# Performance work log

Hardware: AMD Instinct MI355X
Metric: run time of the kernel (lower is better)

## Reference

```python
import jax, jax.numpy as jnp
import numpy as np

DIM = 512
HEADS = 8
DIM_HEAD = 64
HIDDEN = HEADS * DIM_HEAD  # 512
B = 4
L = 2048
SCALE = DIM_HEAD ** -0.5


def setup_inputs() -> dict:
    key = jax.random.key(0)
    k1, k2, k3, k4 = jax.random.split(key, 4)
    x = jax.random.normal(k1, (B, DIM, L), dtype=jnp.float32)
    # Conv1d with kernel_size=1 == pointwise matmul over channels; store as [out, in]
    w_qkv = jax.random.normal(k2, (HIDDEN * 3, DIM), dtype=jnp.float32) * (DIM ** -0.5)
    w_out = jax.random.normal(k3, (DIM, HIDDEN), dtype=jnp.float32) * (HIDDEN ** -0.5)
    b_out = jax.random.normal(k4, (DIM,), dtype=jnp.float32) * 0.01
    return {"x": x, "w_qkv": w_qkv, "w_out": w_out, "b_out": b_out}


def reference(x, w_qkv, w_out, b_out):
    # x: [B, dim, L]
    qkv = jnp.einsum('oi,bil->bol', w_qkv, x)           # [B, 3*hidden, L]
    q, k, v = jnp.split(qkv, 3, axis=1)                  # each [B, hidden, L]

    def to_heads(t):
        # 'b (h c) l -> b h l c'
        return t.reshape(t.shape[0], HEADS, DIM_HEAD, t.shape[-1]).transpose(0, 1, 3, 2)

    q = to_heads(q) * SCALE                              # [B, H, L, c]
    k = to_heads(k)
    v = to_heads(v)

    attn = jax.nn.softmax(jnp.einsum('bhqc,bhkc->bhqk', q, k), axis=-1)  # [B,H,L,L]
    o = jnp.einsum('bhqk,bhkc->bhqc', attn, v)           # [B, H, L, c]
    o = o.transpose(0, 1, 3, 2).reshape(o.shape[0], HIDDEN, o.shape[2] if False else L)
    # 'b h c l -> b (h c) l' done via transpose+reshape above
    out = jnp.einsum('oi,bil->bol', w_out, o) + b_out[None, :, None]
    return out
```

## Files before the change

kernel.cpp:

```cpp
#include <hip/hip_runtime.h>

typedef unsigned short u16;
typedef __bf16 bf16x8 __attribute__((ext_vector_type(8)));
typedef float f32x4 __attribute__((ext_vector_type(4)));

#define B_ 4
#define L_ 2048
#define LOG2E 1.44269504088896340736f
#define HSTRIDE ((size_t)L_ * 64)

__device__ __forceinline__ u16 f2bf(float f) {
    unsigned u = __float_as_uint(f);
    u += 0x7fff + ((u >> 16) & 1);
    return (u16)(u >> 16);
}

__device__ __forceinline__ unsigned pk2(float a, float b) {
    return __builtin_amdgcn_perm(__float_as_uint(b), __float_as_uint(a), 0x07060302u);
}

__device__ __forceinline__ f32x4 mfma16(bf16x8 a, bf16x8 b, f32x4 c) {
    return __builtin_amdgcn_mfma_f32_16x16x32_bf16(a, b, c, 0, 0, 0);
}

__device__ __forceinline__ void async16(const u16* g, u16* l) {
    __builtin_amdgcn_global_load_lds(
        (const __attribute__((address_space(1))) u16*)g,
        (__attribute__((address_space(3))) u16*)l, 16, 0, 0);
}

__global__ __launch_bounds__(256) void convert_f32_bf16(const float* __restrict__ in,
                                                        u16* __restrict__ out, int n) {
    int i = (blockIdx.x * 256 + threadIdx.x) * 4;
    if (i < n) {
        float4 f = *(const float4*)(in + i);
        ushort4 r;
        r.x = f2bf(f.x); r.y = f2bf(f.y); r.z = f2bf(f.z); r.w = f2bf(f.w);
        *(ushort4*)(out + i) = r;
    }
}

__global__ __launch_bounds__(256) void transpose_x(const float* __restrict__ x,
                                                   u16* __restrict__ xbt) {
    __shared__ u16 T[64][66];
    int b  = blockIdx.z;
    int i0 = blockIdx.y * 64;
    int l0 = blockIdx.x * 64;
    int t  = threadIdx.x;
    int c  = t & 63, r4 = t >> 6;
    const float* xb = x + ((size_t)b * 512 + i0) * 2048 + l0;
#pragma unroll
    for (int r = r4; r < 64; r += 4) T[r][c] = f2bf(xb[(size_t)r * 2048 + c]);
    __syncthreads();
    u16* ob = xbt + ((size_t)b * 2048 + l0) * 512 + i0;
#pragma unroll
    for (int r = r4; r < 64; r += 4) ob[(size_t)r * 512 + c] = T[c][r];
}

__global__ __launch_bounds__(256, 2) void qkv_gemm(const u16* __restrict__ xbt,
                                                   const u16* __restrict__ wq,
                                                   u16* __restrict__ qkv) {
    __shared__ u16 smem[16384];
    u16* As = smem;
    u16* Bs = smem + 8192;
    int b  = blockIdx.z;
    int m0 = blockIdx.x * 128;
    int n0 = blockIdx.y * 128;
    int tid = threadIdx.x;
    int lane = tid & 63, wid = tid >> 6;
    int quad = lane >> 4, n15 = lane & 15;
    const u16* Abase = xbt + ((size_t)b * L_ + m0) * 512;
    const u16* Bbase = wq + (size_t)n0 * 512;
    int mw = (wid & 1) * 64, nw = (wid >> 1) * 64;
    f32x4 acc[4][4] = {};
    for (int k0 = 0; k0 < 512; k0 += 64) {
        __syncthreads();
#pragma unroll
        for (int c = 0; c < 4; ++c) {
            int off = wid * 2048 + c * 512 + lane * 8;
            int row = off >> 6, col = off & 63;
            async16(Abase + (size_t)row * 512 + k0 + col, As + wid * 2048 + c * 512);
            async16(Bbase + (size_t)row * 512 + k0 + col, Bs + wid * 2048 + c * 512);
        }
        __syncthreads();
#pragma unroll
        for (int ks = 0; ks < 2; ++ks) {
            bf16x8 af[4], bfr[4];
#pragma unroll
            for (int i = 0; i < 4; ++i)
                af[i] = *(const bf16x8*)&As[(mw + i * 16 + n15) * 64 + ks * 32 + quad * 8];
#pragma unroll
            for (int j = 0; j < 4; ++j)
                bfr[j] = *(const bf16x8*)&Bs[(nw + j * 16 + n15) * 64 + ks * 32 + quad * 8];
#pragma unroll
            for (int i = 0; i < 4; ++i)
#pragma unroll
                for (int j = 0; j < 4; ++j)
                    acc[i][j] = mfma16(af[i], bfr[j], acc[i][j]);
        }
    }
    if (n0 < 512) {
#pragma unroll
        for (int i = 0; i < 4; ++i) {
#pragma unroll
            for (int j = 0; j < 4; ++j) {
                int o = n0 + nw + j * 16 + n15;
                int h = (o >> 6) & 7, cc = o & 63;
                u16* dst = qkv + ((size_t)b * 3 * 8 + h) * HSTRIDE + cc;
#pragma unroll
                for (int r = 0; r < 4; ++r) {
                    int l = m0 + mw + i * 16 + quad * 4 + r;
                    dst[(size_t)l * 64] = f2bf(acc[i][j][r] * (0.125f * LOG2E));
                }
            }
        }
    } else if (n0 < 1024) {
#pragma unroll
        for (int i = 0; i < 4; ++i) {
            int tile = (m0 + mw + i * 16) >> 4;
#pragma unroll
            for (int j = 0; j < 4; ++j) {
                int o = n0 + nw + j * 16 + n15;
                int h = (o >> 6) & 7, c = o & 63;
                int ks_k = c >> 5, qk = (c >> 3) & 3, jj = c & 7;
                u16* dst = qkv + (((size_t)b * 3 + 1) * 8 + h) * HSTRIDE
                         + ((size_t)tile * 2 + ks_k) * 512 + qk * 128 + jj;
#pragma unroll
                for (int r = 0; r < 4; ++r) {
                    int n15k = quad * 4 + r;
                    dst[n15k * 8] = f2bf(acc[i][j][r]);
                }
            }
        }
    } else {
        int kt = m0 >> 7;
        u16* Vf = qkv + ((size_t)b * 3 + 2) * 8 * HSTRIDE;
#pragma unroll
        for (int i = 0; i < 4; ++i) {
            int L0 = mw + i * 16;
            int ks2 = (L0 >> 5) & 3;
            int r3 = ((L0 >> 3) + (quad >> 1)) & 3;
#pragma unroll
            for (int j = 0; j < 4; ++j) {
                int oo = (n0 - 1024) + nw + j * 16 + n15;
                int h = oo >> 6, c = oo & 63;
                ushort4 pk;
                pk.x = f2bf(acc[i][j][0]); pk.y = f2bf(acc[i][j][1]);
                pk.z = f2bf(acc[i][j][2]); pk.w = f2bf(acc[i][j][3]);
                *(ushort4*)&Vf[(size_t)h * HSTRIDE + kt * 8192 + ks2 * 2048
                               + (c >> 4) * 512 + r3 * 128 + n15 * 8 + (quad & 1) * 4] = pk;
            }
        }
    }
}

__global__ __launch_bounds__(256, 4) void attn_kernel(const u16* __restrict__ qkv,
                                                      u16* __restrict__ o2) {
    __shared__ u16 Ps[4 * 32 * 68];
    __shared__ float Ls[4][32];
    int bh = blockIdx.y;
    int b = bh >> 3, h = bh & 7;
    int q0 = blockIdx.x * 32;
    int tid = threadIdx.x, lane = tid & 63, wid = tid >> 6;
    int quad = lane >> 4, n15 = lane & 15;
    const u16* Qp = qkv + (((size_t)b * 3 + 0) * 8 + h) * HSTRIDE;
    const u16* Kf = qkv + (((size_t)b * 3 + 1) * 8 + h) * HSTRIDE;
    const u16* Vf = qkv + (((size_t)b * 3 + 2) * 8 + h) * HSTRIDE;
    u16* Pw = Ps + wid * (32 * 68);

    bf16x8 aq[2][2];
#pragma unroll
    for (int mf = 0; mf < 2; ++mf)
#pragma unroll
        for (int ks = 0; ks < 2; ++ks)
            aq[mf][ks] = *(const bf16x8*)
                &Qp[(size_t)(q0 + mf * 16 + n15) * 64 + ks * 32 + quad * 8];

    f32x4 oacc[2][4] = {};
    float lsumT[2] = {0.f, 0.f};

    for (int it = 0; it < 8; ++it) {
        int tile0 = wid * 32 + it * 4;
#pragma unroll
        for (int nf = 0; nf < 4; ++nf) {
            const u16* kb = Kf + (size_t)(tile0 + nf) * 1024;
            bf16x8 ak0 = *(const bf16x8*)&kb[lane * 8];
            bf16x8 ak1 = *(const bf16x8*)&kb[512 + lane * 8];
#pragma unroll
            for (int mf = 0; mf < 2; ++mf) {
                f32x4 sT = {};
                sT = mfma16(ak0, aq[mf][0], sT);
                sT = mfma16(ak1, aq[mf][1], sT);
                float p0 = __builtin_amdgcn_exp2f(sT[0]);
                float p1 = __builtin_amdgcn_exp2f(sT[1]);
                float p2 = __builtin_amdgcn_exp2f(sT[2]);
                float p3 = __builtin_amdgcn_exp2f(sT[3]);
                lsumT[mf] += (p0 + p1) + (p2 + p3);
                uint2 pw;
                pw.x = pk2(p0, p1);
                pw.y = pk2(p2, p3);
                *(uint2*)&Pw[(mf * 16 + n15) * 68 + nf * 16 + quad * 4] = pw;
            }
        }
#pragma unroll
        for (int sub = 0; sub < 2; ++sub) {
            bf16x8 pa[2];
#pragma unroll
            for (int mf = 0; mf < 2; ++mf)
                pa[mf] = *(const bf16x8*)&Pw[(mf * 16 + n15) * 68 + sub * 32 + quad * 8];
            const u16* vbb = Vf + (size_t)(wid * 16 + it * 2 + sub) * 2048;
#pragma unroll
            for (int nf2 = 0; nf2 < 4; ++nf2) {
                bf16x8 vb = *(const bf16x8*)&vbb[nf2 * 512 + lane * 8];
#pragma unroll
                for (int mf = 0; mf < 2; ++mf)
                    oacc[mf][nf2] = mfma16(pa[mf], vb, oacc[mf][nf2]);
            }
        }
    }

#pragma unroll
    for (int mf = 0; mf < 2; ++mf) {
        float s = lsumT[mf];
        s += __shfl_xor(s, 16, 64);
        s += __shfl_xor(s, 32, 64);
        Ls[wid][mf * 16 + n15] = s;
    }
    float* Ored = (float*)Ps;
#pragma unroll
    for (int mf = 0; mf < 2; ++mf) {
        __syncthreads();
        float* Od = Ored + wid * (16 * 68);
#pragma unroll
        for (int nf2 = 0; nf2 < 4; ++nf2)
#pragma unroll
            for (int r = 0; r < 4; ++r)
                Od[(quad * 4 + r) * 68 + nf2 * 16 + n15] = oacc[mf][nf2][r];
        __syncthreads();
        int row = tid >> 4, c0 = (tid & 15) * 4;
        float4 a0 = *(float4*)&Ored[0 * 1088 + row * 68 + c0];
        float4 a1 = *(float4*)&Ored[1 * 1088 + row * 68 + c0];
        float4 a2 = *(float4*)&Ored[2 * 1088 + row * 68 + c0];
        float4 a3 = *(float4*)&Ored[3 * 1088 + row * 68 + c0];
        float inv = 1.0f / (Ls[0][mf * 16 + row] + Ls[1][mf * 16 + row]
                          + Ls[2][mf * 16 + row] + Ls[3][mf * 16 + row]);
        ushort4 ov;
        ov.x = f2bf((a0.x + a1.x + a2.x + a3.x) * inv);
        ov.y = f2bf((a0.y + a1.y + a2.y + a3.y) * inv);
        ov.z = f2bf((a0.z + a1.z + a2.z + a3.z) * inv);
        ov.w = f2bf((a0.w + a1.w + a2.w + a3.w) * inv);
        *(ushort4*)&o2[((size_t)b * L_ + q0 + mf * 16 + row) * 512 + h * 64 + c0] = ov;
    }
}

__global__ __launch_bounds__(256, 2) void out_gemm(const u16* __restrict__ wo,
                                                   const u16* __restrict__ o2,
                                                   const float* __restrict__ bout,
                                                   float* __restrict__ out) {
    __shared__ u16 As[8192], Bs[8192];
    int b  = blockIdx.z;
    int m0 = blockIdx.y * 128;
    int n0 = blockIdx.x * 128;
    int tid = threadIdx.x, lane = tid & 63, wid = tid >> 6;
    int quad = lane >> 4, n15 = lane & 15;
    const u16* Abase = wo + (size_t)m0 * 512;
    const u16* Bbase = o2 + ((size_t)b * L_ + n0) * 512;
    int mw = (wid & 1) * 64, nw = (wid >> 1) * 64;
    f32x4 acc[4][4] = {};
    for (int k0 = 0; k0 < 512; k0 += 64) {
        __syncthreads();
#pragma unroll
        for (int c = 0; c < 4; ++c) {
            int off = wid * 2048 + c * 512 + lane * 8;
            int row = off >> 6, col = off & 63;
            async16(Abase + (size_t)row * 512 + k0 + col, As + wid * 2048 + c * 512);
            async16(Bbase + (size_t)row * 512 + k0 + col, Bs + wid * 2048 + c * 512);
        }
        __syncthreads();
#pragma unroll
        for (int ks = 0; ks < 2; ++ks) {
            bf16x8 af[4], bfr[4];
#pragma unroll
            for (int i = 0; i < 4; ++i)
                af[i] = *(const bf16x8*)&As[(mw + i * 16 + n15) * 64 + ks * 32 + quad * 8];
#pragma unroll
            for (int j = 0; j < 4; ++j)
                bfr[j] = *(const bf16x8*)&Bs[(nw + j * 16 + n15) * 64 + ks * 32 + quad * 8];
#pragma unroll
            for (int i = 0; i < 4; ++i)
#pragma unroll
                for (int j = 0; j < 4; ++j)
                    acc[i][j] = mfma16(af[i], bfr[j], acc[i][j]);
        }
    }
#pragma unroll
    for (int i = 0; i < 4; ++i) {
#pragma unroll
        for (int r = 0; r < 4; ++r) {
            int o_ = m0 + mw + i * 16 + quad * 4 + r;
            float bias = bout[o_];
            float* dst = out + ((size_t)b * 512 + o_) * L_ + n0;
#pragma unroll
            for (int j = 0; j < 4; ++j) dst[nw + j * 16 + n15] = acc[i][j][r] + bias;
        }
    }
}

#define OFF_XBT  ((size_t)0)
#define OFF_WQKV (OFF_XBT + (size_t)B_ * L_ * 512)
#define OFF_WOUT (OFF_WQKV + (size_t)1536 * 512)
#define OFF_QKV  (OFF_WOUT + (size_t)512 * 512)
#define OFF_O2   (OFF_QKV + (size_t)3 * B_ * 8 * L_ * 64)

extern "C" void kernel_launch(void* const* d_in, const int* in_sizes, int n_in,
                              void* d_out, int out_size, void* d_ws, size_t ws_size,
                              hipStream_t stream) {
    (void)in_sizes; (void)n_in; (void)out_size; (void)ws_size;
    const float* x    = (const float*)d_in[0];
    const float* wqkv = (const float*)d_in[1];
    const float* wout = (const float*)d_in[2];
    const float* bout = (const float*)d_in[3];
    float* out = (float*)d_out;
    u16* ws = (u16*)d_ws;
    u16* xbt   = ws + OFF_XBT;
    u16* wqkvb = ws + OFF_WQKV;
    u16* woutb = ws + OFF_WOUT;
    u16* qkv   = ws + OFF_QKV;
    u16* o2    = ws + OFF_O2;

    convert_f32_bf16<<<768, 256, 0, stream>>>(wqkv, wqkvb, 1536 * 512);
    convert_f32_bf16<<<256, 256, 0, stream>>>(wout, woutb, 512 * 512);
    transpose_x<<<dim3(32, 8, 4), 256, 0, stream>>>(x, xbt);
    qkv_gemm<<<dim3(16, 12, 4), 256, 0, stream>>>(xbt, wqkvb, qkv);
    attn_kernel<<<dim3(64, 32), 256, 0, stream>>>(qkv, o2);
    out_gemm<<<dim3(16, 4, 4), 256, 0, stream>>>(woutb, o2, bout, out);
}
```

Before: 181.5 us.

## Stage Q/K epilogue through LDS, compute row sums via MFMA, shrink out_gemm tiles

The QKV GEMM epilogue for Q and K now stages the bf16 tile in shared memory and writes it back with 16-byte coalesced stores instead of scattered 2-byte stores. The attention kernel drops the per-element scalar row-sum adds and instead gets softmax denominators from an extra MFMA of P against a vector of ones. The output GEMM uses 64-row M tiles, which doubles the grid so more CUs have work. These trade extra LDS traffic, a barrier and extra MFMA work for fewer uncoalesced stores and fewer VALU ops.

```diff
diff --git a/kernel.cpp b/kernel.cpp
--- a/kernel.cpp
+++ b/kernel.cpp
@@ -60,7 +60,7 @@
 __global__ __launch_bounds__(256, 2) void qkv_gemm(const u16* __restrict__ xbt,
                                                    const u16* __restrict__ wq,
                                                    u16* __restrict__ qkv) {
-    __shared__ u16 smem[16384];
+    __shared__ u16 smem[16896];
     u16* As = smem;
     u16* Bs = smem + 8192;
     int b  = blockIdx.z;
@@ -99,38 +99,42 @@
                     acc[i][j] = mfma16(af[i], bfr[j], acc[i][j]);
         }
     }
-    if (n0 < 512) {
-#pragma unroll
-        for (int i = 0; i < 4; ++i) {
-#pragma unroll
-            for (int j = 0; j < 4; ++j) {
-                int o = n0 + nw + j * 16 + n15;
-                int h = (o >> 6) & 7, cc = o & 63;
-                u16* dst = qkv + ((size_t)b * 3 * 8 + h) * HSTRIDE + cc;
-#pragma unroll
-                for (int r = 0; r < 4; ++r) {
-                    int l = m0 + mw + i * 16 + quad * 4 + r;
-                    dst[(size_t)l * 64] = f2bf(acc[i][j][r] * (0.125f * LOG2E));
-                }
-            }
-        }
-    } else if (n0 < 1024) {
-#pragma unroll
-        for (int i = 0; i < 4; ++i) {
-            int tile = (m0 + mw + i * 16) >> 4;
-#pragma unroll
-            for (int j = 0; j < 4; ++j) {
-                int o = n0 + nw + j * 16 + n15;
-                int h = (o >> 6) & 7, c = o & 63;
-                int ks_k = c >> 5, qk = (c >> 3) & 3, jj = c & 7;
-                u16* dst = qkv + (((size_t)b * 3 + 1) * 8 + h) * HSTRIDE
-                         + ((size_t)tile * 2 + ks_k) * 512 + qk * 128 + jj;
-#pragma unroll
-                for (int r = 0; r < 4; ++r) {
-                    int n15k = quad * 4 + r;
-                    dst[n15k * 8] = f2bf(acc[i][j][r]);
-                }
-            }
+    if (n0 < 1024) {
+        __syncthreads();
+        u16* T = smem;
+        float sc = (n0 < 512) ? (0.125f * LOG2E) : 1.0f;
+#pragma unroll
+        for (int i = 0; i < 4; ++i)
+#pragma unroll
+            for (int j = 0; j < 4; ++j)
+#pragma unroll
+                for (int r = 0; r < 4; ++r)
+                    T[(mw + i * 16 + quad * 4 + r) * 132 + (nw + j * 16 + n15)] =
+                        f2bf(acc[i][j][r] * sc);
+        __syncthreads();
+        int t = (n0 < 512) ? 0 : 1;
+        int h0 = (n0 >> 6) & 7;
+        u16* plane = qkv + (((size_t)b * 3 + t) * 8 + h0) * HSTRIDE + (size_t)m0 * 64;
+#pragma unroll
+        for (int it = 0; it < 8; ++it) {
+            int flat = it * 2048 + tid * 8;
+            int h_loc = flat >> 13;
+            int remh = flat & 8191;
+            int src;
+            if (t == 0) {
+                int l_loc = remh >> 6, cc = remh & 63;
+                src = l_loc * 132 + h_loc * 64 + cc;
+            } else {
+                int tile_loc = remh >> 10;
+                int remt = remh & 1023;
+                int ks_ = remt >> 9, qk = (remt >> 7) & 3, n15k = (remt >> 3) & 15;
+                src = (tile_loc * 16 + n15k) * 132 + h_loc * 64 + ks_ * 32 + qk * 8;
+            }
+            ushort4 lo = *(const ushort4*)&T[src];
+            ushort4 hi = *(const ushort4*)&T[src + 4];
+            u16* dst = plane + (size_t)h_loc * HSTRIDE + remh;
+            *(ushort4*)dst = lo;
+            *(ushort4*)(dst + 4) = hi;
         }
     } else {
         int kt = m0 >> 7;
@@ -168,6 +172,10 @@
     const u16* Vf = qkv + (((size_t)b * 3 + 2) * 8 + h) * HSTRIDE;
     u16* Pw = Ps + wid * (32 * 68);
 
+    bf16x8 vones;
+#pragma unroll
+    for (int z = 0; z < 8; ++z) vones[z] = (__bf16)1.0f;
+
     bf16x8 aq[2][2];
 #pragma unroll
     for (int mf = 0; mf < 2; ++mf)
@@ -177,7 +185,7 @@
                 &Qp[(size_t)(q0 + mf * 16 + n15) * 64 + ks * 32 + quad * 8];
 
     f32x4 oacc[2][4] = {};
-    float lsumT[2] = {0.f, 0.f};
+    f32x4 osum[2] = {};
 
     for (int it = 0; it < 8; ++it) {
         int tile0 = wid * 32 + it * 4;
@@ -195,7 +203,6 @@
                 float p1 = __builtin_amdgcn_exp2f(sT[1]);
                 float p2 = __builtin_amdgcn_exp2f(sT[2]);
                 float p3 = __builtin_amdgcn_exp2f(sT[3]);
-                lsumT[mf] += (p0 + p1) + (p2 + p3);
                 uint2 pw;
                 pw.x = pk2(p0, p1);
                 pw.y = pk2(p2, p3);
@@ -206,8 +213,10 @@
         for (int sub = 0; sub < 2; ++sub) {
             bf16x8 pa[2];
 #pragma unroll
-            for (int mf = 0; mf < 2; ++mf)
+            for (int mf = 0; mf < 2; ++mf) {
                 pa[mf] = *(const bf16x8*)&Pw[(mf * 16 + n15) * 68 + sub * 32 + quad * 8];
+                osum[mf] = mfma16(pa[mf], vones, osum[mf]);
+            }
             const u16* vbb = Vf + (size_t)(wid * 16 + it * 2 + sub) * 2048;
 #pragma unroll
             for (int nf2 = 0; nf2 < 4; ++nf2) {
@@ -220,12 +229,10 @@
     }
 
 #pragma unroll
-    for (int mf = 0; mf < 2; ++mf) {
-        float s = lsumT[mf];
-        s += __shfl_xor(s, 16, 64);
-        s += __shfl_xor(s, 32, 64);
-        Ls[wid][mf * 16 + n15] = s;
-    }
+    for (int mf = 0; mf < 2; ++mf)
+#pragma unroll
+        for (int r = 0; r < 4; ++r)
+            Ls[wid][mf * 16 + quad * 4 + r] = osum[mf][r];
     float* Ored = (float*)Ps;
 #pragma unroll
     for (int mf = 0; mf < 2; ++mf) {
@@ -257,44 +264,49 @@
                                                    const u16* __restrict__ o2,
                                                    const float* __restrict__ bout,
                                                    float* __restrict__ out) {
-    __shared__ u16 As[8192], Bs[8192];
+    __shared__ u16 As[4096], Bs[8192];
     int b  = blockIdx.z;
-    int m0 = blockIdx.y * 128;
+    int m0 = blockIdx.y * 64;
     int n0 = blockIdx.x * 128;
     int tid = threadIdx.x, lane = tid & 63, wid = tid >> 6;
     int quad = lane >> 4, n15 = lane & 15;
     const u16* Abase = wo + (size_t)m0 * 512;
     const u16* Bbase = o2 + ((size_t)b * L_ + n0) * 512;
-    int mw = (wid & 1) * 64, nw = (wid >> 1) * 64;
-    f32x4 acc[4][4] = {};
+    int mw = (wid & 1) * 32, nw = (wid >> 1) * 64;
+    f32x4 acc[2][4] = {};
     for (int k0 = 0; k0 < 512; k0 += 64) {
         __syncthreads();
+#pragma unroll
+        for (int a = 0; a < 2; ++a) {
+            int off = wid * 1024 + a * 512 + lane * 8;
+            int row = off >> 6, col = off & 63;
+            async16(Abase + (size_t)row * 512 + k0 + col, As + off);
+        }
 #pragma unroll
         for (int c = 0; c < 4; ++c) {
             int off = wid * 2048 + c * 512 + lane * 8;
             int row = off >> 6, col = off & 63;
-            async16(Abase + (size_t)row * 512 + k0 + col, As + wid * 2048 + c * 512);
-            async16(Bbase + (size_t)row * 512 + k0 + col, Bs + wid * 2048 + c * 512);
+            async16(Bbase + (size_t)row * 512 + k0 + col, Bs + off);
         }
         __syncthreads();
 #pragma unroll
         for (int ks = 0; ks < 2; ++ks) {
-            bf16x8 af[4], bfr[4];
-#pragma unroll
-            for (int i = 0; i < 4; ++i)
+            bf16x8 af[2], bfr[4];
+#pragma unroll
+            for (int i = 0; i < 2; ++i)
                 af[i] = *(const bf16x8*)&As[(mw + i * 16 + n15) * 64 + ks * 32 + quad * 8];
 #pragma unroll
             for (int j = 0; j < 4; ++j)
                 bfr[j] = *(const bf16x8*)&Bs[(nw + j * 16 + n15) * 64 + ks * 32 + quad * 8];
 #pragma unroll
-            for (int i = 0; i < 4; ++i)
+            for (int i = 0; i < 2; ++i)
 #pragma unroll
                 for (int j = 0; j < 4; ++j)
                     acc[i][j] = mfma16(af[i], bfr[j], acc[i][j]);
         }
     }
 #pragma unroll
-    for (int i = 0; i < 4; ++i) {
+    for (int i = 0; i < 2; ++i) {
 #pragma unroll
         for (int r = 0; r < 4; ++r) {
             int o_ = m0 + mw + i * 16 + quad * 4 + r;
@@ -333,5 +345,5 @@
     transpose_x<<<dim3(32, 8, 4), 256, 0, stream>>>(x, xbt);
     qkv_gemm<<<dim3(16, 12, 4), 256, 0, stream>>>(xbt, wqkvb, qkv);
     attn_kernel<<<dim3(64, 32), 256, 0, stream>>>(qkv, o2);
-    out_gemm<<<dim3(16, 4, 4), 256, 0, stream>>>(woutb, o2, bout, out);
-}
+    out_gemm<<<dim3(16, 8, 4), 256, 0, stream>>>(woutb, o2, bout, out);
+}
```

Result: faster. 173.2 us (-4.6%).
